# Performance work log

Hardware: AMD Instinct MI355X
Metric: run time of the kernel (lower is better)

Reference implementation:

```python
import jax, jax.numpy as jnp
import numpy as np

N = 50000        # nodes
E = 800000       # edges
R = 8            # relations
G = 64           # g_dim
H1 = 64          # h1_dim
H2 = 32          # h2_dim (per-head for transformer, output for sage)
HEADS = 4
EPS = 1e-5       # BatchNorm eps


def setup_inputs() -> dict:
    key = jax.random.key(0)
    ks = jax.random.split(key, 16)
    def rn(k, shape, scale=0.05):
        return jax.random.normal(k, shape, dtype=jnp.float32) * scale
    return {
        "node_features": jax.random.normal(ks[0], (N, G), dtype=jnp.float32),
        "node_type": jax.random.randint(ks[1], (N,), 0, 3),
        "edge_index": jax.random.randint(ks[2], (2, E), 0, N),
        "edge_type": jax.random.randint(ks[3], (E,), 0, R),
        # RGCNConv params (per-relation weight + root weight + bias)
        "rgcn_w": rn(ks[4], (R, G, H1)),
        "rgcn_root": rn(ks[5], (G, H1)),
        "rgcn_bias": jnp.zeros((H1,), jnp.float32),
        "bn1_g": jnp.ones((H1,), jnp.float32),
        "bn1_b": jnp.zeros((H1,), jnp.float32),
        # TransformerConv params (q/k/v projections + skip)
        "wq": rn(ks[6], (H1, HEADS * H2)), "bq": jnp.zeros((HEADS * H2,), jnp.float32),
        "wk": rn(ks[7], (H1, HEADS * H2)), "bk": jnp.zeros((HEADS * H2,), jnp.float32),
        "wv": rn(ks[8], (H1, HEADS * H2)), "bv": jnp.zeros((HEADS * H2,), jnp.float32),
        "wskip": rn(ks[9], (H1, HEADS * H2)), "bskip": jnp.zeros((HEADS * H2,), jnp.float32),
        "bn2_g": jnp.ones((HEADS * H2,), jnp.float32),
        "bn2_b": jnp.zeros((HEADS * H2,), jnp.float32),
        # SAGEConv params (lin_l on aggregated neighbors has bias; lin_r on root has none)
        "sage_wl": rn(ks[10], (HEADS * H2, H2)), "sage_bl": jnp.zeros((H2,), jnp.float32),
        "sage_wr": rn(ks[11], (HEADS * H2, H2)),
        "bn3_g": jnp.ones((H2,), jnp.float32),
        "bn3_b": jnp.zeros((H2,), jnp.float32),
    }


def _bn(x, g, b):
    # BatchNorm1d in training mode: biased batch statistics over nodes
    m = x.mean(0)
    v = x.var(0)
    return g * (x - m) * jax.lax.rsqrt(v + EPS) + b


def _match(res, d):
    # F.pad(res, (0, d - c)): pads with zeros if d > c, truncates if d < c
    c = res.shape[1]
    if d > c:
        return jnp.pad(res, ((0, 0), (0, d - c)))
    return res[:, :d]


def _forward(node_features, rgcn_w, rgcn_root, rgcn_bias, bn1_g, bn1_b,
             wq, bq, wk, bk, wv, bv, wskip, bskip, bn2_g, bn2_b,
             sage_wl, sage_bl, sage_wr, bn3_g, bn3_b,
             edge_index, edge_type):
    src, dst = edge_index[0], edge_index[1]
    x = node_features
    residual = x

    # ---- RGCNConv: per-relation transform, per-relation mean aggregation, sum over relations ----
    xr = jnp.einsum('nf,rfh->nrh', x, rgcn_w)            # [N,R,H1]
    msg = xr[src, edge_type]                              # [E,H1]
    seg = dst * R + edge_type                             # segment per (node, relation)
    sums = jax.ops.segment_sum(msg, seg, num_segments=N * R)
    cnt = jax.ops.segment_sum(jnp.ones((E,), msg.dtype), seg, num_segments=N * R)
    agg = (sums / jnp.maximum(cnt, 1.0)[:, None]).reshape(N, R, H1).sum(1)
    h = agg + x @ rgcn_root + rgcn_bias
    h = jax.nn.leaky_relu(_bn(h, bn1_g, bn1_b))
    x = h + _match(residual, h.shape[1])
    residual = x

    # ---- TransformerConv: edge softmax attention, concat heads, + skip projection ----
    q = (x @ wq + bq).reshape(N, HEADS, H2)
    k = (x @ wk + bk).reshape(N, HEADS, H2)
    v = (x @ wv + bv).reshape(N, HEADS, H2)
    logits = (q[dst] * k[src]).sum(-1) / jnp.sqrt(jnp.float32(H2))  # [E,HEADS]
    mx = jax.ops.segment_max(logits, dst, num_segments=N)
    ex = jnp.exp(logits - mx[dst])
    den = jax.ops.segment_sum(ex, dst, num_segments=N)
    alpha = ex / jnp.maximum(den[dst], 1e-16)
    out = jax.ops.segment_sum(alpha[:, :, None] * v[src], dst, num_segments=N)
    h = out.reshape(N, HEADS * H2) + x @ wskip + bskip
    h = jax.nn.leaky_relu(_bn(h, bn2_g, bn2_b))
    x = h + _match(residual, h.shape[1])
    residual = x

    # ---- SAGEConv: mean neighbor aggregation + root transform ----
    nsum = jax.ops.segment_sum(x[src], dst, num_segments=N)
    ncnt = jax.ops.segment_sum(jnp.ones((E,), x.dtype), dst, num_segments=N)
    nmean = nsum / jnp.maximum(ncnt, 1.0)[:, None]
    h = nmean @ sage_wl + sage_bl + x @ sage_wr
    h = jax.nn.leaky_relu(_bn(h, bn3_g, bn3_b))
    return h + _match(residual, h.shape[1])


def reference(node_features, node_type, edge_index, edge_type,
              rgcn_w, rgcn_root, rgcn_bias, bn1_g, bn1_b,
              wq, bq, wk, bk, wv, bv, wskip, bskip, bn2_g, bn2_b,
              sage_wl, sage_bl, sage_wr, bn3_g, bn3_b):
    # node_type is unused by the original forward
    return _forward(node_features, rgcn_w, rgcn_root, rgcn_bias, bn1_g, bn1_b,
                    wq, bq, wk, bk, wv, bv, wskip, bskip, bn2_g, bn2_b,
                    sage_wl, sage_bl, sage_wr, bn3_g, bn3_b,
                    edge_index, edge_type)
```

## Files before the change

kernel.cpp:

```cpp
#include <hip/hip_runtime.h>
#include <stdint.h>

#define NN 50000
#define NE 800000
#define NE8 (NE/8)
#define NR (NN*8)
#define SCAN_BS 512
#define NB2 782
#define INV_N (1.0f/50000.0f)
#define BN_EPS 1e-5f

typedef unsigned short ushort_t;
typedef unsigned char uchar_t;
typedef short bf16x8 __attribute__((ext_vector_type(8)));
typedef float f32x4 __attribute__((ext_vector_type(4)));
typedef float f32x2 __attribute__((ext_vector_type(2)));

__device__ __forceinline__ ushort_t f2bf(float f){
    unsigned int u = __float_as_uint(f);
    u += 0x7FFFu + ((u >> 16) & 1u);
    return (ushort_t)(u >> 16);
}
__device__ __forceinline__ float bf2f(ushort_t h){ return __uint_as_float(((unsigned int)h) << 16); }
__device__ __forceinline__ float bflo(unsigned int u){ return __uint_as_float(u << 16); }
__device__ __forceinline__ float bfhi(unsigned int u){ return __uint_as_float(u & 0xFFFF0000u); }

__device__ __forceinline__ unsigned int f4_to_fp8(float a, float b, float c, float d){
    int v = __builtin_amdgcn_cvt_pk_fp8_f32(a, b, 0, false);
    v = __builtin_amdgcn_cvt_pk_fp8_f32(c, d, v, true);
    return (unsigned int)v;
}
__device__ __forceinline__ void fp8_to_f4(unsigned int u, float& a, float& b, float& c, float& d){
    f32x2 lo = __builtin_amdgcn_cvt_pk_f32_fp8(u, false);
    f32x2 hi = __builtin_amdgcn_cvt_pk_f32_fp8(u, true);
    a = lo.x; b = lo.y; c = hi.x; d = hi.y;
}

__global__ void k_prep(const float* __restrict__ nf,
                       const float* __restrict__ rgcn_w, const float* __restrict__ root,
                       const float* __restrict__ wq, const float* __restrict__ wk,
                       const float* __restrict__ wv, const float* __restrict__ wsk,
                       const float* __restrict__ bq, const float* __restrict__ bk,
                       const float* __restrict__ bv, const float* __restrict__ bsk,
                       const float* __restrict__ wl, const float* __restrict__ wr,
                       const int* __restrict__ ei, const int* __restrict__ et,
                       int* __restrict__ deg, uint2* __restrict__ sr,
                       ushort_t* __restrict__ xb, uchar_t* __restrict__ xb8,
                       ushort_t* __restrict__ Wcat,
                       ushort_t* __restrict__ Wt2, float* __restrict__ bcat,
                       ushort_t* __restrict__ Wsage){
    int i = blockIdx.x*256 + threadIdx.x;
    if (i < NE8){
        const int4* dp = (const int4*)(ei + NE);
        const int4* rp = (const int4*)et;
        int4 d0 = dp[i*2], d1 = dp[i*2 + 1];
        int4 r0 = rp[i*2], r1 = rp[i*2 + 1];
        int sg[8];
        sg[0] = d0.x*8 + r0.x; sg[1] = d0.y*8 + r0.y;
        sg[2] = d0.z*8 + r0.z; sg[3] = d0.w*8 + r0.w;
        sg[4] = d1.x*8 + r1.x; sg[5] = d1.y*8 + r1.y;
        sg[6] = d1.z*8 + r1.z; sg[7] = d1.w*8 + r1.w;
        int rk[8];
#pragma unroll
        for (int u = 0; u < 8; ++u) rk[u] = atomicAdd(&deg[sg[u]], 1);
        uint2* o = sr + (size_t)i*8;
#pragma unroll
        for (int u = 0; u < 8; ++u){
            uint2 ov; ov.x = (unsigned)sg[u]; ov.y = (unsigned)rk[u];
            o[u] = ov;
        }
        return;
    }
    int ii = i - NE8;
    const int NXB = NN*16;
    if (ii < NXB){
        float4 v = ((const float4*)nf)[ii];
        ushort4 h;
        h.x = f2bf(v.x); h.y = f2bf(v.y); h.z = f2bf(v.z); h.w = f2bf(v.w);
        ((ushort4*)xb)[ii] = h;
        ((unsigned int*)xb8)[ii] = f4_to_fp8(v.x, v.y, v.z, v.w);
        return;
    }
    int j = ii - NXB;
    if (j < 64*576){
        int h = j / 576, k = j - h*576;
        float v = (k < 512) ? rgcn_w[(size_t)k*64 + h] : root[(size_t)(k-512)*64 + h];
        Wcat[j] = f2bf(v);
    } else if (j < 64*576 + 512*64){
        int jj = j - 64*576;
        int c = jj >> 6, k = jj & 63;
        int mt = c >> 7, cc = c & 127;
        const float* W = (mt==0)?wq:(mt==1)?wk:(mt==2)?wv:wsk;
        Wt2[jj] = f2bf(W[(size_t)k*128 + cc]);
    } else if (j < 64*576 + 512*64 + 512){
        int c = j - (64*576 + 512*64);
        int mt = c >> 7, cc = c & 127;
        const float* B = (mt==0)?bq:(mt==1)?bk:(mt==2)?bv:bsk;
        bcat[c] = B[cc];
    } else if (j < 64*576 + 512*64 + 512 + 32*256){
        int jj = j - (64*576 + 512*64 + 512);
        int c = jj >> 8, k = jj & 255;
        float v = (k < 128) ? wr[(size_t)k*32 + c] : wl[(size_t)(k-128)*32 + c];
        Wsage[jj] = f2bf(v);
    }
}

__global__ void k_scan1(const int* __restrict__ deg, int* __restrict__ tmp, int* __restrict__ bsum){
    __shared__ int s[SCAN_BS];
    int t = threadIdx.x;
    int i = blockIdx.x*SCAN_BS + t;
    s[t] = (i < NR) ? deg[i] : 0;
    __syncthreads();
    for (int off = 1; off < SCAN_BS; off <<= 1){
        int add = (t >= off) ? s[t-off] : 0;
        __syncthreads();
        s[t] += add;
        __syncthreads();
    }
    if (i < NR) tmp[i] = s[t];
    if (t == SCAN_BS-1) bsum[blockIdx.x] = s[t];
}

__global__ void k_scan3(const int* __restrict__ tmp, const int* __restrict__ bsum, int* __restrict__ rs){
    __shared__ int sacc[256];
    int B = blockIdx.x;
    int b = B >> 1;
    int t = threadIdx.x;
    int acc = 0;
    for (int g = t; g < b; g += 256) acc += bsum[g];
    sacc[t] = acc;
    __syncthreads();
    for (int off2 = 128; off2 > 0; off2 >>= 1){
        if (t < off2) sacc[t] += sacc[t + off2];
        __syncthreads();
    }
    int off = sacc[0];
    int i = B*256 + t;
    if (i < NR){
        rs[i+1] = tmp[i] + off;
        if (i == 0) rs[0] = 0;
    }
}

__global__ void k_fill(const int* __restrict__ ei, const uint2* __restrict__ sr,
                       const int* __restrict__ rs, int* __restrict__ csr){
    int e = blockIdx.x*256 + threadIdx.x;
    if (e < NE){
        uint2 s = sr[e];
        csr[rs[s.x] + (int)s.y] = ei[e];
    }
}

__global__ __launch_bounds__(256) void rgcn_fused(const ushort_t* __restrict__ xb,
                                                  const uchar_t* __restrict__ xb8,
                                                  const int* __restrict__ rs,
                                                  const int* __restrict__ csr,
                                                  const ushort_t* __restrict__ Wcat,
                                                  const float* __restrict__ bias,
                                                  float* __restrict__ h1pre,
                                                  float* __restrict__ part1){
    __shared__ ushort_t Ml[8*520];
    int w = threadIdx.x >> 6, lane = threadIdx.x & 63;
    int quad = lane >> 4, l4 = lane & 15;
    int row0 = blockIdx.x * 8;
    int n0 = row0 + w*2;
    int rsel = (lane < 9 ? lane : 8);
    int rb = rs[n0*8 + rsel];
    int eb0 = __shfl(rb, 0);
    int dg0 = __shfl(rb, 8) - eb0;
    int idx = (lane < dg0) ? csr[eb0 + lane] : 0;
    for (int j = 0; j < 2; ++j){
        int lrow = (w*2 + j)*520;
        int ebase = __shfl(rb, 0);
        int enext = __shfl(rb, 8);
        int rb_next = 0, idxn = 0;
        if (j < 1){
            rb_next = rs[(n0 + j + 1)*8 + rsel];
            idxn = csr[min(enext + lane, NE - 1)];
        }
        int e0a = __shfl(rb, 2*quad);
        int e1a = __shfl(rb, 2*quad + 1);
        int e2a = __shfl(rb, 2*quad + 2);
        int oa = e0a - ebase;
        int la = e1a - e0a, lb = e2a - e1a;
        int tot = la + lb;
        int fastN = min(tot, max(64 - oa, 0));
        int ml = fastN;
        ml = max(ml, __shfl_xor(ml, 16));
        ml = max(ml, __shfl_xor(ml, 32));
        f32x2 aA0 = {0.f,0.f}, aA1 = {0.f,0.f};
        f32x2 aB0 = {0.f,0.f}, aB1 = {0.f,0.f};
        for (int i = 0; i < ml; i += 4){
            unsigned int uX[4];
#pragma unroll
            for (int u = 0; u < 4; ++u){
                int jj = i + u;
                int t = __shfl(idx, (oa + jj) & 63);
                t = (jj < fastN) ? t : 0;
                uX[u] = *(const unsigned int*)(xb8 + (size_t)t*64 + l4*4);
            }
#pragma unroll
            for (int u = 0; u < 4; ++u){
                int jj = i + u;
                unsigned int a = (jj < fastN) ? uX[u] : 0u;
                f32x2 lo = __builtin_amdgcn_cvt_pk_f32_fp8(a, false);
                f32x2 hi = __builtin_amdgcn_cvt_pk_f32_fp8(a, true);
                if (jj < la){ aA0 += lo; aA1 += hi; }
                else        { aB0 += lo; aB1 += hi; }
            }
        }
        for (int jj = min(la, fastN); jj < la; ++jj){
            int t = csr[e0a + jj];
            unsigned int a = *(const unsigned int*)(xb8 + (size_t)t*64 + l4*4);
            aA0 += __builtin_amdgcn_cvt_pk_f32_fp8(a, false);
            aA1 += __builtin_amdgcn_cvt_pk_f32_fp8(a, true);
        }
        for (int jj = max(la, fastN); jj < tot; ++jj){
            int t = csr[e0a + jj];
            unsigned int b = *(const unsigned int*)(xb8 + (size_t)t*64 + l4*4);
            aB0 += __builtin_amdgcn_cvt_pk_f32_fp8(b, false);
            aB1 += __builtin_amdgcn_cvt_pk_f32_fp8(b, true);
        }
        float inva = 1.f / fmaxf((float)la, 1.f);
        float invb = 1.f / fmaxf((float)lb, 1.f);
        ushort4 oA, oB;
        oA.x = f2bf(aA0.x*inva); oA.y = f2bf(aA0.y*inva); oA.z = f2bf(aA1.x*inva); oA.w = f2bf(aA1.y*inva);
        oB.x = f2bf(aB0.x*invb); oB.y = f2bf(aB0.y*invb); oB.z = f2bf(aB1.x*invb); oB.w = f2bf(aB1.y*invb);
        *(ushort4*)&Ml[lrow + (2*quad)*64 + l4*4] = oA;
        *(ushort4*)&Ml[lrow + (2*quad + 1)*64 + l4*4] = oB;
        if (j < 1){
            rb = rb_next;
            int ebn = __shfl(rb, 0);
            int dgn = __shfl(rb, 8) - ebn;
            idx = (lane < dgn) ? idxn : 0;
        }
    }
    __syncthreads();
    int m = l4;
    int m8 = m & 7;
    f32x4 acc = {};
#pragma unroll
    for (int kt = 0; kt < 18; ++kt){
        int kk = kt*32 + quad*8;
        bf16x8 a;
        if (kt < 16) a = *(const bf16x8*)&Ml[m8*520 + kk];
        else         a = *(const bf16x8*)(xb + (size_t)(row0 + m8)*64 + (kk - 512));
        bf16x8 b = *(const bf16x8*)(Wcat + (size_t)(w*16 + m)*576 + kk);
        acc = __builtin_amdgcn_mfma_f32_16x16x32_bf16(a, b, acc, 0, 0, 0);
    }
    int col = w*16 + m;
    float bz = bias[col];
    float s = 0.f, q = 0.f;
#pragma unroll
    for (int i = 0; i < 4; ++i){
        int r = quad*4 + i;
        if (r < 8){
            float y = acc[i] + bz;
            h1pre[(size_t)(row0 + r)*64 + col] = y;
            s += y; q += y*y;
        }
    }
    s += __shfl_xor(s, 16); q += __shfl_xor(q, 16);
    s += __shfl_xor(s, 32); q += __shfl_xor(q, 32);
    if (quad == 0){
        float* pg = part1 + (blockIdx.x & 31)*128;
        atomicAdd(&pg[col], s);
        atomicAdd(&pg[64 + col], q);
    }
}

#define QS 132
#define BS 68
__global__ __launch_bounds__(256) void gemm_qkvs(const float* __restrict__ h1pre,
                                                 const float* __restrict__ nf,
                                                 const float* __restrict__ part1,
                                                 const float* __restrict__ g1, const float* __restrict__ b1,
                                                 const ushort_t* __restrict__ Wt2,
                                                 const float* __restrict__ bcat,
                                                 ushort_t* __restrict__ qb,
                                                 uchar_t* __restrict__ kb8,
                                                 uchar_t* __restrict__ vb8,
                                                 ushort_t* __restrict__ sb){
    __shared__ ushort_t Bs[256*BS];
    __shared__ ushort_t pl[4][16*QS];
    __shared__ float sred[128];
    int w = threadIdx.x >> 6, lane = threadIdx.x & 63;
    int m = lane & 15, quad = lane >> 4;
    int r0 = blockIdx.x*64 + w*16;
    int row = r0 + m;
    {
        int t = threadIdx.x;
        if (t < 128){
            float acc = 0.f;
#pragma unroll
            for (int g = 0; g < 32; ++g) acc += part1[g*128 + t];
            sred[t] = acc;
        }
    }
    __syncthreads();
    bf16x8 afrag[2];
#pragma unroll
    for (int kt = 0; kt < 2; ++kt){
        int db = kt*32 + quad*8;
        bf16x8 f = (bf16x8){0,0,0,0,0,0,0,0};
        if (row < NN){
            float4 h0 = *(const float4*)(h1pre + (size_t)row*64 + db);
            float4 h1 = *(const float4*)(h1pre + (size_t)row*64 + db + 4);
            float4 n0 = *(const float4*)(nf + (size_t)row*64 + db);
            float4 n1 = *(const float4*)(nf + (size_t)row*64 + db + 4);
            float4 ga = *(const float4*)(g1 + db);
            float4 gb_ = *(const float4*)(g1 + db + 4);
            float4 ba = *(const float4*)(b1 + db);
            float4 bb_ = *(const float4*)(b1 + db + 4);
            float hh[8] = {h0.x,h0.y,h0.z,h0.w,h1.x,h1.y,h1.z,h1.w};
            float nn[8] = {n0.x,n0.y,n0.z,n0.w,n1.x,n1.y,n1.z,n1.w};
            float GG[8] = {ga.x,ga.y,ga.z,ga.w,gb_.x,gb_.y,gb_.z,gb_.w};
            float BB[8] = {ba.x,ba.y,ba.z,ba.w,bb_.x,bb_.y,bb_.z,bb_.w};
#pragma unroll
            for (int e = 0; e < 8; ++e){
                float mm = sred[db + e] * INV_N;
                float vv = sred[64 + db + e] * INV_N - mm*mm;
                float A = rsqrtf(fmaxf(vv, 0.f) + BN_EPS) * GG[e];
                float C = BB[e] - mm * A;
                float y = fmaf(hh[e], A, C);
                y = (y >= 0.f) ? y : 0.01f*y;
                f[e] = (short)f2bf(y + nn[e]);
            }
        }
        afrag[kt] = f;
    }
    for (int cg = 0; cg < 2; ++cg){
        __syncthreads();
        {
            int t = threadIdx.x;
            const ushort_t* wsrc = Wt2 + (size_t)cg*256*64;
#pragma unroll
            for (int u0 = 0; u0 < 8; ++u0){
                int u = u0*256 + t;
                int r = u >> 3, c8 = (u & 7)*8;
                *(uint4*)&Bs[r*BS + c8] = *(const uint4*)(wsrc + u*8);
            }
        }
        __syncthreads();
        f32x4 acc[16] = {};
#pragma unroll
        for (int kt = 0; kt < 2; ++kt){
            int kk = kt*32 + quad*8;
#pragma unroll
            for (int ct = 0; ct < 16; ++ct){
                bf16x8 b = *(const bf16x8*)&Bs[(size_t)(ct*16 + m)*BS + kk];
                acc[ct] = __builtin_amdgcn_mfma_f32_16x16x32_bf16(afrag[kt], b, acc[ct], 0, 0, 0);
            }
        }
#pragma unroll
        for (int ct = 0; ct < 8; ++ct){
            int g = cg*256 + ct*16 + m;
            float bz = bcat[g];
            int cc = g & 127;
#pragma unroll
            for (int i = 0; i < 4; ++i)
                pl[w][(quad*4 + i)*QS + cc] = f2bf(acc[ct][i] + bz);
        }
        if (cg == 0){
#pragma unroll
            for (int t = 0; t < 4; ++t){
                int u = t*64 + lane;
                int r = u >> 4, c = (u & 15)*8;
                int gr = r0 + r;
                if (gr < NN) *(uint4*)(qb + (size_t)gr*128 + c) = *(const uint4*)&pl[w][r*QS + c];
            }
        } else {
#pragma unroll
            for (int t = 0; t < 4; ++t){
                int u = t*64 + lane;
                int r = u >> 4, c = (u & 15)*8;
                int gr = r0 + r;
                if (gr < NN){
                    uint4 vv4 = *(const uint4*)&pl[w][r*QS + c];
                    uint2 o;
                    o.x = f4_to_fp8(bflo(vv4.x), bfhi(vv4.x), bflo(vv4.y), bfhi(vv4.y));
                    o.y = f4_to_fp8(bflo(vv4.z), bfhi(vv4.z), bflo(vv4.w), bfhi(vv4.w));
                    *(uint2*)(vb8 + (size_t)gr*128 + c) = o;
                }
            }
        }
#pragma unroll
        for (int ct = 8; ct < 16; ++ct){
            int g = cg*256 + ct*16 + m;
            float bz = bcat[g];
            int cc = g & 127;
#pragma unroll
            for (int i = 0; i < 4; ++i)
                pl[w][(quad*4 + i)*QS + cc] = f2bf(acc[ct][i] + bz);
        }
        if (cg == 0){
#pragma unroll
            for (int t = 0; t < 4; ++t){
                int u = t*64 + lane;
                int r = u >> 4, c = (u & 15)*8;
                int gr = r0 + r;
                if (gr < NN){
                    uint4 kk4 = *(const uint4*)&pl[w][r*QS + c];
                    uint2 o;
                    o.x = f4_to_fp8(bflo(kk4.x), bfhi(kk4.x), bflo(kk4.y), bfhi(kk4.y));
                    o.y = f4_to_fp8(bflo(kk4.z), bfhi(kk4.z), bflo(kk4.w), bfhi(kk4.w));
                    *(uint2*)(kb8 + (size_t)gr*128 + c) = o;
                }
            }
        } else {
#pragma unroll
            for (int t = 0; t < 4; ++t){
                int u = t*64 + lane;
                int r = u >> 4, c = (u & 15)*8;
                int gr = r0 + r;
                if (gr < NN) *(uint4*)(sb + (size_t)gr*128 + c) = *(const uint4*)&pl[w][r*QS + c];
            }
        }
    }
}

__global__ void k_red2(const float* __restrict__ part1, const float* __restrict__ part2,
                       float* __restrict__ bns){
    int t = threadIdx.x;
    float acc = 0.f;
    for (int g = 0; g < 64; ++g) acc += part2[g*256 + t];
    bns[128 + t] = acc;
    if (t < 128){
        float a1 = 0.f;
        for (int g = 0; g < 32; ++g) a1 += part1[g*128 + t];
        bns[t] = a1;
    }
}

__global__ __launch_bounds__(256) void sage_gemm(const ushort_t* __restrict__ x2b,
                                                 const ushort_t* __restrict__ nmeanb,
                                                 const ushort_t* __restrict__ Wsage,
                                                 const float* __restrict__ bl,
                                                 float* __restrict__ h3,
                                                 float* __restrict__ part3){
    int wv = threadIdx.x >> 6, lane = threadIdx.x & 63;
    int r0 = blockIdx.x*64 + wv*16;
    int m = lane & 15, quad = lane >> 4;
    int row = r0 + m;
    f32x4 acc[2] = {};
#pragma unroll
    for (int kt = 0; kt < 8; ++kt){
        int kk = kt*32 + quad*8;
        bf16x8 a;
        if (row < NN){
            const ushort_t* ap = (kt < 4) ? (x2b + (size_t)row*128 + kk)
                                          : (nmeanb + (size_t)row*128 + (kk - 128));
            a = *(const bf16x8*)ap;
        } else {
            a = (bf16x8){0,0,0,0,0,0,0,0};
        }
#pragma unroll
        for (int ct = 0; ct < 2; ++ct){
            bf16x8 b = *(const bf16x8*)(Wsage + (size_t)(ct*16 + m)*256 + kk);
            acc[ct] = __builtin_amdgcn_mfma_f32_16x16x32_bf16(a, b, acc[ct], 0, 0, 0);
        }
    }
    float s[2] = {0.f, 0.f}, q[2] = {0.f, 0.f};
#pragma unroll
    for (int ct = 0; ct < 2; ++ct){
        int col = ct*16 + m;
        float bz = bl[col];
#pragma unroll
        for (int i = 0; i < 4; ++i){
            int rr = r0 + quad*4 + i;
            if (rr < NN){
                float y = acc[ct][i] + bz;
                h3[(size_t)rr*32 + col] = y;
                s[ct] += y; q[ct] += y*y;
            }
        }
    }
#pragma unroll
    for (int ct = 0; ct < 2; ++ct){
        s[ct] += __shfl_xor(s[ct], 16); q[ct] += __shfl_xor(q[ct], 16);
        s[ct] += __shfl_xor(s[ct], 32); q[ct] += __shfl_xor(q[ct], 32);
    }
    if (quad == 0){
        float* pg = part3 + (blockIdx.x & 3)*64;
#pragma unroll
        for (int ct = 0; ct < 2; ++ct){
            int col = ct*16 + m;
            atomicAdd(&pg[col], s[ct]);
            atomicAdd(&pg[32 + col], q[ct]);
        }
    }
}

__device__ __forceinline__ float bn_leaky(float z, float m, float rsv, float g, float b){
    float y = (z - m) * rsv * g + b;
    return y >= 0.f ? y : 0.01f * y;
}

__global__ void bn_apply2(const float* __restrict__ h2, const float* __restrict__ h1pre,
                          const float* __restrict__ nf,
                          const float* __restrict__ g1, const float* __restrict__ b1,
                          const float* __restrict__ s1, const float* __restrict__ q1,
                          const float* __restrict__ g2, const float* __restrict__ b2,
                          const float* __restrict__ s2, const float* __restrict__ q2,
                          float* __restrict__ x2r, ushort_t* __restrict__ x2b,
                          uchar_t* __restrict__ x28){
    int i = blockIdx.x*256 + threadIdx.x;
    if (i >= NN*128) return;
    int n = i >> 7, c = i & 127;
    float m2 = s2[c] * INV_N;
    float v2 = q2[c] * INV_N - m2*m2;
    float rsv2 = rsqrtf(fmaxf(v2, 0.f) + BN_EPS);
    float val = bn_leaky(h2[i], m2, rsv2, g2[c], b2[c]);
    if (c < 64){
        float m1 = s1[c] * INV_N;
        float v1 = q1[c] * INV_N - m1*m1;
        float rsv1 = rsqrtf(fmaxf(v1, 0.f) + BN_EPS);
        val += bn_leaky(h1pre[(size_t)n*64 + c], m1, rsv1, g1[c], b1[c]) + nf[(size_t)n*64 + c];
    }
    if (c < 32) x2r[(size_t)n*32 + c] = val;
    x2b[i] = f2bf(val);
    int p = __builtin_amdgcn_cvt_pk_fp8_f32(val, val, 0, false);
    x28[i] = (uchar_t)(p & 0xFF);
}

__global__ void bn_apply3(const float* __restrict__ h3, const float* __restrict__ x2r,
                          const float* __restrict__ g, const float* __restrict__ b,
                          const float* __restrict__ part3,
                          float* __restrict__ out){
    int i = blockIdx.x*256 + threadIdx.x;
    if (i >= NN*32) return;
    int c = i & 31;
    float s = 0.f, q = 0.f;
#pragma unroll
    for (int gg = 0; gg < 4; ++gg){
        s += part3[gg*64 + c];
        q += part3[gg*64 + 32 + c];
    }
    float m = s * INV_N;
    float v = q * INV_N - m*m;
    float rsv = rsqrtf(fmaxf(v, 0.f) + BN_EPS);
    out[i] = bn_leaky(h3[i], m, rsv, g[c], b[c]) + x2r[i];
}

__global__ __launch_bounds__(256) void attn_kernel(const ushort_t* __restrict__ qb,
                                                   const uchar_t* __restrict__ kb8,
                                                   const uchar_t* __restrict__ vb8,
                                                   const ushort_t* __restrict__ sb,
                                                   const int* __restrict__ rs,
                                                   const int* __restrict__ csr,
                                                   float* __restrict__ h2,
                                                   float* __restrict__ part2){
    __shared__ float sm[2][4][128];
    int w = threadIdx.x >> 6, lane = threadIdx.x & 63;
    int n = blockIdx.x*4 + w;
    int half = lane >> 5, l5 = lane & 31;
    int e0 = rs[n*8], e1 = rs[n*8 + 8];
    int deg = e1 - e0;
    uint2 qu = *(const uint2*)(qb + (size_t)n*128 + l5*4);
    uint2 sbv = *(const uint2*)(sb + (size_t)n*128 + l5*4);
    float q0 = bflo(qu.x), q1 = bfhi(qu.x), q2 = bflo(qu.y), q3 = bfhi(qu.y);
    const float scale = 0.17677669529663687f;
    int idx = 0;
    if (lane < deg) idx = csr[e0 + lane];
    int dcap = min(deg, 64);
    int nt = (dcap + 7) >> 3;
    float den = 0.f, a0 = 0.f, a1 = 0.f, a2 = 0.f, a3 = 0.f;
    for (int t = 0; t < nt; ++t){
        int i2 = t*8 + half*4;
        int j0 = i2, j1 = i2+1, j2 = i2+2, j3 = i2+3;
        bool v0 = j0 < dcap, v1 = j1 < dcap, v2 = j2 < dcap, v3 = j3 < dcap;
        int s0 = __shfl(idx, j0 & 63); s0 = v0 ? s0 : 0;
        int s1 = __shfl(idx, j1 & 63); s1 = v1 ? s1 : 0;
        int s2 = __shfl(idx, j2 & 63); s2 = v2 ? s2 : 0;
        int s3 = __shfl(idx, j3 & 63); s3 = v3 ? s3 : 0;
        unsigned int ku0 = *(const unsigned int*)(kb8 + (size_t)s0*128 + l5*4);
        unsigned int ku1 = *(const unsigned int*)(kb8 + (size_t)s1*128 + l5*4);
        unsigned int ku2 = *(const unsigned int*)(kb8 + (size_t)s2*128 + l5*4);
        unsigned int ku3 = *(const unsigned int*)(kb8 + (size_t)s3*128 + l5*4);
        unsigned int vu0 = *(const unsigned int*)(vb8 + (size_t)s0*128 + l5*4);
        unsigned int vu1 = *(const unsigned int*)(vb8 + (size_t)s1*128 + l5*4);
        unsigned int vu2 = *(const unsigned int*)(vb8 + (size_t)s2*128 + l5*4);
        unsigned int vu3 = *(const unsigned int*)(vb8 + (size_t)s3*128 + l5*4);
        float ka, kb_, kc, kd;
        fp8_to_f4(ku0, ka, kb_, kc, kd);
        float p0 = q0*ka + q1*kb_ + q2*kc + q3*kd;
        fp8_to_f4(ku1, ka, kb_, kc, kd);
        float p1 = q0*ka + q1*kb_ + q2*kc + q3*kd;
        fp8_to_f4(ku2, ka, kb_, kc, kd);
        float p2 = q0*ka + q1*kb_ + q2*kc + q3*kd;
        fp8_to_f4(ku3, ka, kb_, kc, kd);
        float p3 = q0*ka + q1*kb_ + q2*kc + q3*kd;
        p0 += __shfl_xor(p0, 1); p1 += __shfl_xor(p1, 1); p2 += __shfl_xor(p2, 1); p3 += __shfl_xor(p3, 1);
        p0 += __shfl_xor(p0, 2); p1 += __shfl_xor(p1, 2); p2 += __shfl_xor(p2, 2); p3 += __shfl_xor(p3, 2);
        p0 += __shfl_xor(p0, 4); p1 += __shfl_xor(p1, 4); p2 += __shfl_xor(p2, 4); p3 += __shfl_xor(p3, 4);
        float w0 = v0 ? __expf(p0 * scale) : 0.f;
        float w1 = v1 ? __expf(p1 * scale) : 0.f;
        float w2 = v2 ? __expf(p2 * scale) : 0.f;
        float w3 = v3 ? __expf(p3 * scale) : 0.f;
        den += w0 + w1 + w2 + w3;
        float va, vb_, vc, vd;
        fp8_to_f4(vu0, va, vb_, vc, vd);
        a0 = fmaf(w0, va, a0); a1 = fmaf(w0, vb_, a1); a2 = fmaf(w0, vc, a2); a3 = fmaf(w0, vd, a3);
        fp8_to_f4(vu1, va, vb_, vc, vd);
        a0 = fmaf(w1, va, a0); a1 = fmaf(w1, vb_, a1); a2 = fmaf(w1, vc, a2); a3 = fmaf(w1, vd, a3);
        fp8_to_f4(vu2, va, vb_, vc, vd);
        a0 = fmaf(w2, va, a0); a1 = fmaf(w2, vb_, a1); a2 = fmaf(w2, vc, a2); a3 = fmaf(w2, vd, a3);
        fp8_to_f4(vu3, va, vb_, vc, vd);
        a0 = fmaf(w3, va, a0); a1 = fmaf(w3, vb_, a1); a2 = fmaf(w3, vc, a2); a3 = fmaf(w3, vd, a3);
    }
    for (int e = 64 + half; e < deg; e += 2){
        int s = csr[e0 + e];
        unsigned int ku = *(const unsigned int*)(kb8 + (size_t)s*128 + l5*4);
        unsigned int vu = *(const unsigned int*)(vb8 + (size_t)s*128 + l5*4);
        float ka, kb_, kc, kd;
        fp8_to_f4(ku, ka, kb_, kc, kd);
        float p = q0*ka + q1*kb_ + q2*kc + q3*kd;
        p += __shfl_xor(p, 1);
        p += __shfl_xor(p, 2);
        p += __shfl_xor(p, 4);
        float wg = __expf(p * scale);
        den += wg;
        float va, vb_, vc, vd;
        fp8_to_f4(vu, va, vb_, vc, vd);
        a0 = fmaf(wg, va, a0); a1 = fmaf(wg, vb_, a1); a2 = fmaf(wg, vc, a2); a3 = fmaf(wg, vd, a3);
    }
    den += __shfl_xor(den, 32);
    a0 += __shfl_xor(a0, 32); a1 += __shfl_xor(a1, 32);
    a2 += __shfl_xor(a2, 32); a3 += __shfl_xor(a3, 32);
    float inv = (den > 0.f) ? 1.f/den : 0.f;
    float o0 = bflo(sbv.x) + a0*inv;
    float o1 = bfhi(sbv.x) + a1*inv;
    float o2 = bflo(sbv.y) + a2*inv;
    float o3 = bfhi(sbv.y) + a3*inv;
    if (half == 0){
        float4 o; o.x = o0; o.y = o1; o.z = o2; o.w = o3;
        *(float4*)(h2 + (size_t)n*128 + l5*4) = o;
        float4 t; t.x = o0; t.y = o1; t.z = o2; t.w = o3;
        *(float4*)&sm[0][w][l5*4] = t;
    } else {
        float4 t; t.x = o0*o0; t.y = o1*o1; t.z = o2*o2; t.w = o3*o3;
        *(float4*)&sm[1][w][l5*4] = t;
    }
    __syncthreads();
    {
        int t = threadIdx.x;
        int st = t >> 7, c = t & 127;
        float v = sm[st][0][c] + sm[st][1][c] + sm[st][2][c] + sm[st][3][c];
        atomicAdd(&part2[(blockIdx.x & 63)*256 + st*128 + c], v);
    }
}

__global__ __launch_bounds__(256) void sage_agg(const uchar_t* __restrict__ x28,
                                                const int* __restrict__ rs,
                                                const int* __restrict__ csr,
                                                ushort_t* __restrict__ nmeanb){
    int w = threadIdx.x >> 6, lane = threadIdx.x & 63;
    int n = blockIdx.x*4 + w;
    if (n >= NN) return;
    int half = lane >> 5, l5 = lane & 31;
    int e0 = rs[n*8], e1 = rs[n*8 + 8];
    int deg = e1 - e0;
    int idx = 0;
    if (lane < deg) idx = csr[e0 + lane];
    int dcap = min(deg, 64);
    int nt = (dcap + 7) >> 3;
    f32x2 A0 = {0.f,0.f}, A1 = {0.f,0.f};
    for (int t = 0; t < nt; ++t){
        int i2 = t*8 + half*4;
        int j0 = i2, j1 = i2+1, j2 = i2+2, j3 = i2+3;
        bool v0 = j0 < dcap, v1 = j1 < dcap, v2 = j2 < dcap, v3 = j3 < dcap;
        int s0 = __shfl(idx, j0 & 63); s0 = v0 ? s0 : 0;
        int s1 = __shfl(idx, j1 & 63); s1 = v1 ? s1 : 0;
        int s2 = __shfl(idx, j2 & 63); s2 = v2 ? s2 : 0;
        int s3 = __shfl(idx, j3 & 63); s3 = v3 ? s3 : 0;
        unsigned int u0 = *(const unsigned int*)(x28 + (size_t)s0*128 + l5*4);
        unsigned int u1 = *(const unsigned int*)(x28 + (size_t)s1*128 + l5*4);
        unsigned int u2 = *(const unsigned int*)(x28 + (size_t)s2*128 + l5*4);
        unsigned int u3 = *(const unsigned int*)(x28 + (size_t)s3*128 + l5*4);
        u0 = v0 ? u0 : 0u; u1 = v1 ? u1 : 0u;
        u2 = v2 ? u2 : 0u; u3 = v3 ? u3 : 0u;
        A0 += __builtin_amdgcn_cvt_pk_f32_fp8(u0, false);
        A1 += __builtin_amdgcn_cvt_pk_f32_fp8(u0, true);
        A0 += __builtin_amdgcn_cvt_pk_f32_fp8(u1, false);
        A1 += __builtin_amdgcn_cvt_pk_f32_fp8(u1, true);
        A0 += __builtin_amdgcn_cvt_pk_f32_fp8(u2, false);
        A1 += __builtin_amdgcn_cvt_pk_f32_fp8(u2, true);
        A0 += __builtin_amdgcn_cvt_pk_f32_fp8(u3, false);
        A1 += __builtin_amdgcn_cvt_pk_f32_fp8(u3, true);
    }
    for (int e = 64 + half; e < deg; e += 2){
        int s = csr[e0 + e];
        unsigned int u = *(const unsigned int*)(x28 + (size_t)s*128 + l5*4);
        A0 += __builtin_amdgcn_cvt_pk_f32_fp8(u, false);
        A1 += __builtin_amdgcn_cvt_pk_f32_fp8(u, true);
    }
    float a0 = A0.x, a1 = A0.y, a2 = A1.x, a3 = A1.y;
    a0 += __shfl_xor(a0, 32); a1 += __shfl_xor(a1, 32);
    a2 += __shfl_xor(a2, 32); a3 += __shfl_xor(a3, 32);
    if (half == 0){
        float inv = 1.f / fmaxf((float)deg, 1.f);
        ushort4 o;
        o.x = f2bf(a0*inv); o.y = f2bf(a1*inv); o.z = f2bf(a2*inv); o.w = f2bf(a3*inv);
        *(ushort4*)(nmeanb + (size_t)n*128 + l5*4) = o;
    }
}

extern "C" void kernel_launch(void* const* d_in, const int* in_sizes, int n_in,
                              void* d_out, int out_size, void* d_ws, size_t ws_size,
                              hipStream_t stream){
    const float* nf      = (const float*)d_in[0];
    const int*   ei      = (const int*)d_in[2];
    const int*   et      = (const int*)d_in[3];
    const float* rgcn_w  = (const float*)d_in[4];
    const float* root    = (const float*)d_in[5];
    const float* rbias   = (const float*)d_in[6];
    const float* bn1g    = (const float*)d_in[7];
    const float* bn1b    = (const float*)d_in[8];
    const float* wq      = (const float*)d_in[9];
    const float* bq      = (const float*)d_in[10];
    const float* wk      = (const float*)d_in[11];
    const float* bk      = (const float*)d_in[12];
    const float* wv      = (const float*)d_in[13];
    const float* bv      = (const float*)d_in[14];
    const float* wsk     = (const float*)d_in[15];
    const float* bsk     = (const float*)d_in[16];
    const float* bn2g    = (const float*)d_in[17];
    const float* bn2b    = (const float*)d_in[18];
    const float* wl      = (const float*)d_in[19];
    const float* bl      = (const float*)d_in[20];
    const float* wr      = (const float*)d_in[21];
    const float* bn3g    = (const float*)d_in[22];
    const float* bn3b    = (const float*)d_in[23];
    float* out = (float*)d_out;

    char* base = (char*)d_ws;
    size_t off = 0;
    auto take = [&](size_t bytes) -> char* {
        char* p = base + off;
        off += (bytes + 255) & ~(size_t)255;
        return p;
    };
    int*      deg    = (int*)take((size_t)NR*4);
    float*    bns    = (float*)take(1024*4);
    float*    part1  = (float*)take(32*128*4);
    float*    part2  = (float*)take(64*256*4);
    float*    part3  = (float*)take(4*64*4);
    char*     zend   = base + off;
    int*      rs     = (int*)take((size_t)(NR+1)*4);
    int*      tmp    = (int*)take((size_t)NR*4);
    int*      bsum   = (int*)take(1024*4);
    uint2*    sr     = (uint2*)take((size_t)NE*8);
    int*      csr    = (int*)take((size_t)NE*4);
    ushort_t* Wcat   = (ushort_t*)take(64*576*2);
    ushort_t* Wt2    = (ushort_t*)take(512*64*2);
    float*    bcat   = (float*)take(512*4);
    ushort_t* Wsage  = (ushort_t*)take(32*256*2);
    ushort_t* xb     = (ushort_t*)take((size_t)NN*64*2);
    uchar_t*  xb8    = (uchar_t*)take((size_t)NN*64);
    float*    h1pre  = (float*)take((size_t)NN*64*4);
    float*    h2     = (float*)take((size_t)NN*128*4);
    float*    x2r    = (float*)take((size_t)NN*32*4);
    ushort_t* sb     = (ushort_t*)take((size_t)NN*128*2);
    char*     bigA   = take((size_t)NN*512*2);
    if (off > ws_size) return;

    ushort_t* qb     = (ushort_t*)(bigA + (size_t)NN*128);
    uchar_t*  vb8    = (uchar_t*)(bigA + (size_t)NN*384);
    uchar_t*  kb8    = (uchar_t*)(bigA + (size_t)NN*640);
    ushort_t* x2b    = (ushort_t*)bigA;
    uchar_t*  x28    = (uchar_t*)(bigA + (size_t)NN*256);
    ushort_t* nmeanb = (ushort_t*)(bigA + (size_t)NN*512);
    float*    h3     = (float*)(bigA + (size_t)NN*768);

    hipMemsetAsync(deg, 0, (size_t)(zend - (char*)deg), stream);

    const int PREP_N = NE8 + NN*16 + 64*576 + 512*64 + 512 + 32*256;
    k_prep <<<(PREP_N+255)/256, 256, 0, stream>>>(nf, rgcn_w, root, wq, wk, wv, wsk,
                                                  bq, bk, bv, bsk, wl, wr,
                                                  ei, et, deg, sr,
                                                  xb, xb8, Wcat, Wt2, bcat, Wsage);
    k_scan1<<<NB2, SCAN_BS, 0, stream>>>(deg, tmp, bsum);
    k_scan3<<<(NR+255)/256, 256, 0, stream>>>(tmp, bsum, rs);
    k_fill <<<(NE+255)/256, 256, 0, stream>>>(ei, sr, rs, csr);

    const int NB4 = (NN + 3) / 4;
    const int NBG = (NN + 63) / 64;

    rgcn_fused<<<NN/8, 256, 0, stream>>>(xb, xb8, rs, csr, Wcat, rbias, h1pre, part1);

    gemm_qkvs<<<NBG, 256, 0, stream>>>(h1pre, nf, part1, bn1g, bn1b,
                                       Wt2, bcat, qb, kb8, vb8, sb);
    attn_kernel<<<NB4, 256, 0, stream>>>(qb, kb8, vb8, sb, rs, csr, h2, part2);
    k_red2<<<1, 256, 0, stream>>>(part1, part2, bns);
    bn_apply2<<<(NN*128+255)/256, 256, 0, stream>>>(h2, h1pre, nf,
                                                    bn1g, bn1b, bns + 0, bns + 64,
                                                    bn2g, bn2b, bns + 128, bns + 256,
                                                    x2r, x2b, x28);

    sage_agg<<<NB4, 256, 0, stream>>>(x28, rs, csr, nmeanb);
    sage_gemm<<<NBG, 256, 0, stream>>>(x2b, nmeanb, Wsage, bl, h3, part3);
    bn_apply3<<<(NN*32+255)/256, 256, 0, stream>>>(h3, x2r, bn3g, bn3b, part3, out);
}
```

Measured before the change: 386.7 us.

## Process 16 rows per RGCN block to fill MFMA tile; vectorize CSR fill

The fused RGCN kernel now aggregates 16 destination nodes per block (4 per wave) instead of 8. This uses all 16 rows of the 16x16 MFMA tile rather than duplicating 8, halves the number of blocks and halves the weight reads per node. Separately, the CSR fill kernel handles four edges per thread with vector loads of the sort keys and source indices. The trade-offs are longer serial aggregation per wave, double the shared memory per block, and 50000/16 must divide exactly.

```diff
diff --git a/kernel.cpp b/kernel.cpp
--- a/kernel.cpp
+++ b/kernel.cpp
@@ -4,6 +4,7 @@
 #define NN 50000
 #define NE 800000
 #define NE8 (NE/8)
+#define NE4 (NE/4)
 #define NR (NN*8)
 #define SCAN_BS 512
 #define NB2 782
@@ -144,10 +145,19 @@
 
 __global__ void k_fill(const int* __restrict__ ei, const uint2* __restrict__ sr,
                        const int* __restrict__ rs, int* __restrict__ csr){
-    int e = blockIdx.x*256 + threadIdx.x;
-    if (e < NE){
-        uint2 s = sr[e];
-        csr[rs[s.x] + (int)s.y] = ei[e];
+    int i = blockIdx.x*256 + threadIdx.x;
+    if (i < NE4){
+        const uint4* sp = (const uint4*)sr;
+        uint4 s01 = sp[i*2], s23 = sp[i*2 + 1];
+        int4 src = ((const int4*)ei)[i];
+        int p0 = rs[s01.x] + (int)s01.y;
+        int p1 = rs[s01.z] + (int)s01.w;
+        int p2 = rs[s23.x] + (int)s23.y;
+        int p3 = rs[s23.z] + (int)s23.w;
+        csr[p0] = src.x;
+        csr[p1] = src.y;
+        csr[p2] = src.z;
+        csr[p3] = src.w;
     }
 }
 
@@ -159,22 +169,22 @@
                                                   const float* __restrict__ bias,
                                                   float* __restrict__ h1pre,
                                                   float* __restrict__ part1){
-    __shared__ ushort_t Ml[8*520];
+    __shared__ ushort_t Ml[16*520];
     int w = threadIdx.x >> 6, lane = threadIdx.x & 63;
     int quad = lane >> 4, l4 = lane & 15;
-    int row0 = blockIdx.x * 8;
-    int n0 = row0 + w*2;
+    int row0 = blockIdx.x * 16;
+    int n0 = row0 + w*4;
     int rsel = (lane < 9 ? lane : 8);
     int rb = rs[n0*8 + rsel];
     int eb0 = __shfl(rb, 0);
     int dg0 = __shfl(rb, 8) - eb0;
     int idx = (lane < dg0) ? csr[eb0 + lane] : 0;
-    for (int j = 0; j < 2; ++j){
-        int lrow = (w*2 + j)*520;
+    for (int j = 0; j < 4; ++j){
+        int lrow = (w*4 + j)*520;
         int ebase = __shfl(rb, 0);
         int enext = __shfl(rb, 8);
         int rb_next = 0, idxn = 0;
-        if (j < 1){
+        if (j < 3){
             rb_next = rs[(n0 + j + 1)*8 + rsel];
             idxn = csr[min(enext + lane, NE - 1)];
         }
@@ -228,7 +238,7 @@
         oB.x = f2bf(aB0.x*invb); oB.y = f2bf(aB0.y*invb); oB.z = f2bf(aB1.x*invb); oB.w = f2bf(aB1.y*invb);
         *(ushort4*)&Ml[lrow + (2*quad)*64 + l4*4] = oA;
         *(ushort4*)&Ml[lrow + (2*quad + 1)*64 + l4*4] = oB;
-        if (j < 1){
+        if (j < 3){
             rb = rb_next;
             int ebn = __shfl(rb, 0);
             int dgn = __shfl(rb, 8) - ebn;
@@ -237,14 +247,13 @@
     }
     __syncthreads();
     int m = l4;
-    int m8 = m & 7;
     f32x4 acc = {};
 #pragma unroll
     for (int kt = 0; kt < 18; ++kt){
         int kk = kt*32 + quad*8;
         bf16x8 a;
-        if (kt < 16) a = *(const bf16x8*)&Ml[m8*520 + kk];
-        else         a = *(const bf16x8*)(xb + (size_t)(row0 + m8)*64 + (kk - 512));
+        if (kt < 16) a = *(const bf16x8*)&Ml[m*520 + kk];
+        else         a = *(const bf16x8*)(xb + (size_t)(row0 + m)*64 + (kk - 512));
         bf16x8 b = *(const bf16x8*)(Wcat + (size_t)(w*16 + m)*576 + kk);
         acc = __builtin_amdgcn_mfma_f32_16x16x32_bf16(a, b, acc, 0, 0, 0);
     }
@@ -253,12 +262,10 @@
     float s = 0.f, q = 0.f;
 #pragma unroll
     for (int i = 0; i < 4; ++i){
-        int r = quad*4 + i;
-        if (r < 8){
-            float y = acc[i] + bz;
-            h1pre[(size_t)(row0 + r)*64 + col] = y;
-            s += y; q += y*y;
-        }
+        int rr = row0 + quad*4 + i;
+        float y = acc[i] + bz;
+        h1pre[(size_t)rr*64 + col] = y;
+        s += y; q += y*y;
     }
     s += __shfl_xor(s, 16); q += __shfl_xor(q, 16);
     s += __shfl_xor(s, 32); q += __shfl_xor(q, 32);
@@ -781,12 +788,12 @@
                                                   xb, xb8, Wcat, Wt2, bcat, Wsage);
     k_scan1<<<NB2, SCAN_BS, 0, stream>>>(deg, tmp, bsum);
     k_scan3<<<(NR+255)/256, 256, 0, stream>>>(tmp, bsum, rs);
-    k_fill <<<(NE+255)/256, 256, 0, stream>>>(ei, sr, rs, csr);
+    k_fill <<<(NE4+255)/256, 256, 0, stream>>>(ei, sr, rs, csr);
 
     const int NB4 = (NN + 3) / 4;
     const int NBG = (NN + 63) / 64;
 
-    rgcn_fused<<<NN/8, 256, 0, stream>>>(xb, xb8, rs, csr, Wcat, rbias, h1pre, part1);
+    rgcn_fused<<<NN/16, 256, 0, stream>>>(xb, xb8, rs, csr, Wcat, rbias, h1pre, part1);
 
     gemm_qkvs<<<NBG, 256, 0, stream>>>(h1pre, nf, part1, bn1g, bn1b,
                                        Wt2, bcat, qb, kb8, vb8, sb);
```

Result: faster. 370.8 us (-4.1%).
